# Kernel optimization log

Hardware: AMD Instinct MI355X
Metric: run time of the kernel (lower is better)

Reference implementation:

```python
import jax, jax.numpy as jnp
import numpy as np
import math

B, S, E, H = 8, 1024, 512, 8
EPS = 1e-5

def _ln(x, g, b):
    mu = jnp.mean(x, axis=-1, keepdims=True)
    var = jnp.mean(jnp.square(x - mu), axis=-1, keepdims=True)
    return (x - mu) * jax.lax.rsqrt(var + EPS) * g + b

def setup_inputs() -> dict:
    key = jax.random.key(0)
    ks = iter(jax.random.split(key, 40))
    def w(shape, scale=0.02):
        return jax.random.normal(next(ks), shape, dtype=jnp.float32) * scale
    inp = {
        'x': jax.random.normal(next(ks), (B, S, E), dtype=jnp.float32),
        'cond': jax.random.normal(next(ks), (B, 1, E), dtype=jnp.float32),
        # AdaLN modulation linears (stored as (in,out))
        'g1w': w((E, E)), 'g1b': jnp.zeros((E,), jnp.float32),
        'be1w': w((E, E)), 'be1b': jnp.zeros((E,), jnp.float32),
        'a1w': w((E, E)), 'a1b': jnp.zeros((E,), jnp.float32),
        'g2w': w((E, E)), 'g2b': jnp.zeros((E,), jnp.float32),
        'be2w': w((E, E)), 'be2b': jnp.zeros((E,), jnp.float32),
        'a2w': w((E, E)), 'a2b': jnp.zeros((E,), jnp.float32),
        # LayerNorm affine
        'ln1g': jnp.ones((E,), jnp.float32), 'ln1b': jnp.zeros((E,), jnp.float32),
        'ln2g': jnp.ones((E,), jnp.float32), 'ln2b': jnp.zeros((E,), jnp.float32),
        # attention projections: each head has width E -> out dim H*E
        'wq': w((E, H * E)), 'bq': jnp.zeros((H * E,), jnp.float32),
        'wk': w((E, H * E)), 'bk': jnp.zeros((H * E,), jnp.float32),
        'wv': w((E, H * E)), 'bv': jnp.zeros((H * E,), jnp.float32),
        'lvw': w((H * E, E)), 'lvb': jnp.zeros((E,), jnp.float32),
        # FFN
        'f1w': w((E, 4 * E)), 'f1b': jnp.zeros((4 * E,), jnp.float32),
        'f2w': w((4 * E, E)), 'f2b': jnp.zeros((E,), jnp.float32),
    }
    return inp

def reference(x, cond, g1w, g1b, be1w, be1b, a1w, a1b, g2w, g2b, be2w, be2b, a2w, a2b,
              ln1g, ln1b, ln2g, ln2b, wq, bq, wk, bk, wv, bv, lvw, lvb, f1w, f1b, f2w, f2b):
    # AdaLN modulation signals, each (B,1,E)
    gamma1 = cond @ g1w + g1b
    beta1 = cond @ be1w + be1b
    alpha1 = cond @ a1w + a1b
    gamma2 = cond @ g2w + g2b
    beta2 = cond @ be2w + be2b
    alpha2 = cond @ a2w + a2b

    y = _ln(x, ln1g, ln1b) * (1.0 + gamma1) + beta1
    q = (y @ wq + bq).reshape(B, S, H, E).transpose(0, 2, 1, 3)  # (B,H,S,E)
    k = (y @ wk + bk).reshape(B, S, H, E).transpose(0, 2, 1, 3)
    v = (y @ wv + bv).reshape(B, S, H, E).transpose(0, 2, 1, 3)
    # NOTE: original scales by sqrt(q.size(2)) == sqrt(seq_len), not head_dim
    scale = 1.0 / math.sqrt(S)
    attn = jax.nn.softmax(jnp.einsum('bhse,bhte->bhst', q, k) * scale, axis=-1)
    o = jnp.einsum('bhst,bhte->bhse', attn, v)  # (B,H,S,E)
    o = o.transpose(0, 2, 1, 3).reshape(B, S, H * E)
    y = x + (o @ lvw + lvb) * alpha1

    z = _ln(y, ln2g, ln2b) * (1.0 + gamma2) + beta2
    z = (jax.nn.relu(z @ f1w + f1b) @ f2w + f2b) * alpha2
    return y + z
```

## Files before the change

### kernel.cpp

```cpp
#include <hip/hip_runtime.h>
#include <hip/hip_bf16.h>

typedef __bf16 bf16_t;
typedef bf16_t bf16x8 __attribute__((ext_vector_type(8)));
typedef bf16_t bf16x4 __attribute__((ext_vector_type(4)));
typedef float f32x4 __attribute__((ext_vector_type(4)));

typedef const __attribute__((address_space(1))) void GV;
typedef __attribute__((address_space(3))) void LV;

__device__ __forceinline__ void gload_lds16(const bf16_t* gsrc, bf16_t* ldst) {
    __builtin_amdgcn_global_load_lds((GV*)gsrc, (LV*)ldst, 16, 0, 0);
}

__global__ __launch_bounds__(256) void wtrans_kernel(const float* __restrict__ in,
                                                     bf16_t* __restrict__ out, int K, int N)
{
    __shared__ float tile[32][33];
    const int n0 = blockIdx.x * 32, k0 = blockIdx.y * 32;
    const int tx = threadIdx.x & 31, ty = threadIdx.x >> 5;
#pragma unroll
    for (int i = 0; i < 32; i += 8)
        tile[ty + i][tx] = in[(long long)(k0 + ty + i) * N + n0 + tx];
    __syncthreads();
#pragma unroll
    for (int i = 0; i < 32; i += 8)
        out[(long long)(n0 + ty + i) * K + k0 + tx] = (bf16_t)tile[tx][ty + i];
}

__global__ __launch_bounds__(256) void modsig_kernel(
    const float* __restrict__ cond,
    const float* __restrict__ w0, const float* __restrict__ w1, const float* __restrict__ w2,
    const float* __restrict__ w3, const float* __restrict__ w4, const float* __restrict__ w5,
    const float* __restrict__ c0, const float* __restrict__ c1, const float* __restrict__ c2,
    const float* __restrict__ c3, const float* __restrict__ c4, const float* __restrict__ c5,
    float* __restrict__ out)
{
    __shared__ float cs[512];
    const int sig = blockIdx.x >> 3, b = blockIdx.x & 7;
    const float* w; const float* bi;
    switch (sig) {
        case 0: w = w0; bi = c0; break;
        case 1: w = w1; bi = c1; break;
        case 2: w = w2; bi = c2; break;
        case 3: w = w3; bi = c3; break;
        case 4: w = w4; bi = c4; break;
        default: w = w5; bi = c5; break;
    }
    for (int i = threadIdx.x; i < 512; i += 256) cs[i] = cond[b * 512 + i];
    __syncthreads();
    for (int n = threadIdx.x; n < 512; n += 256) {
        float s = bi[n];
        for (int i = 0; i < 512; ++i) s = fmaf(cs[i], w[(long long)i * 512 + n], s);
        out[(long long)(sig * 8 + b) * 512 + n] = s;
    }
}

__global__ __launch_bounds__(128) void ln_mod_kernel(
    const float* __restrict__ x, const float* __restrict__ g, const float* __restrict__ be,
    const float* __restrict__ gamma, const float* __restrict__ beta, bf16_t* __restrict__ out)
{
    const int row = blockIdx.x;
    const int b = row >> 10;
    const int t = threadIdx.x;
    const float4 v = reinterpret_cast<const float4*>(x + (long long)row * 512)[t];
    float s = v.x + v.y + v.z + v.w;
    float ss = v.x * v.x + v.y * v.y + v.z * v.z + v.w * v.w;
    for (int o = 32; o; o >>= 1) { s += __shfl_xor(s, o); ss += __shfl_xor(ss, o); }
    __shared__ float red[4];
    if ((t & 63) == 0) { red[t >> 6] = s; red[2 + (t >> 6)] = ss; }
    __syncthreads();
    s = red[0] + red[1]; ss = red[2] + red[3];
    const float mu = s * (1.f / 512.f);
    const float rstd = rsqrtf(ss * (1.f / 512.f) - mu * mu + 1e-5f);
    const float4 gv = reinterpret_cast<const float4*>(g)[t];
    const float4 bv = reinterpret_cast<const float4*>(be)[t];
    const float4 ga = reinterpret_cast<const float4*>(gamma + b * 512)[t];
    const float4 bb = reinterpret_cast<const float4*>(beta + b * 512)[t];
    bf16x4 ov;
    ov[0] = (bf16_t)(((v.x - mu) * rstd * gv.x + bv.x) * (1.f + ga.x) + bb.x);
    ov[1] = (bf16_t)(((v.y - mu) * rstd * gv.y + bv.y) * (1.f + ga.y) + bb.y);
    ov[2] = (bf16_t)(((v.z - mu) * rstd * gv.z + bv.z) * (1.f + ga.z) + bb.z);
    ov[3] = (bf16_t)(((v.w - mu) * rstd * gv.w + bv.w) * (1.f + ga.w) + bb.w);
    reinterpret_cast<bf16x4*>(out + (long long)row * 512)[t] = ov;
}

template <int EPI>
__global__ __launch_bounds__(256) void gemm128_kernel(
    const bf16_t* __restrict__ A, const bf16_t* __restrict__ B,
    const float* __restrict__ bias, void* Cout,
    int M, int N, int K, int lda, int ldb, int ldc)
{
    const int m0 = blockIdx.y * 128, n0 = blockIdx.x * 128;
    const int tid = threadIdx.x, lane = tid & 63, wid = tid >> 6;
    const int wr = wid >> 1, wc = wid & 1;

    __shared__ bf16_t As[4096];
    __shared__ bf16_t Bs[4096];

    f32x4 acc[4][4];
#pragma unroll
    for (int m = 0; m < 4; ++m)
#pragma unroll
        for (int n = 0; n < 4; ++n) acc[m][n] = (f32x4){0.f, 0.f, 0.f, 0.f};

    const int r0 = wid * 16 + (lane >> 2);
    const int lc = (lane & 3) ^ ((lane >> 2) & 3);
    const long long aOff0 = (long long)(m0 + r0) * lda + lc * 8;
    const long long aOff1 = (long long)(m0 + r0 + 64) * lda + lc * 8;
    const long long bOff0 = (long long)(n0 + r0) * ldb + lc * 8;
    const long long bOff1 = (long long)(n0 + r0 + 64) * ldb + lc * 8;
    bf16_t* aDst0 = As + wid * 512;
    bf16_t* aDst1 = As + 2048 + wid * 512;
    bf16_t* bDst0 = Bs + wid * 512;
    bf16_t* bDst1 = Bs + 2048 + wid * 512;

    const int frow = lane & 15, lg = lane >> 4;
    const int pc = lg ^ (frow & 3);

    for (int kt = 0; kt < K; kt += 32) {
        gload_lds16(A + aOff0 + kt, aDst0);
        gload_lds16(A + aOff1 + kt, aDst1);
        gload_lds16(B + bOff0 + kt, bDst0);
        gload_lds16(B + bOff1 + kt, bDst1);
        __syncthreads();
        bf16x8 af[4], bfv[4];
#pragma unroll
        for (int m = 0; m < 4; ++m)
            af[m] = *reinterpret_cast<const bf16x8*>(As + (wr * 64 + m * 16 + frow) * 32 + pc * 8);
#pragma unroll
        for (int n = 0; n < 4; ++n)
            bfv[n] = *reinterpret_cast<const bf16x8*>(Bs + (wc * 64 + n * 16 + frow) * 32 + pc * 8);
        __builtin_amdgcn_s_setprio(1);
#pragma unroll
        for (int m = 0; m < 4; ++m)
#pragma unroll
            for (int n = 0; n < 4; ++n)
                acc[m][n] = __builtin_amdgcn_mfma_f32_16x16x32_bf16(af[m], bfv[n], acc[m][n], 0, 0, 0);
        __builtin_amdgcn_s_setprio(0);
        __syncthreads();
    }

#pragma unroll
    for (int m = 0; m < 4; ++m) {
        const int gm = m0 + wr * 64 + m * 16 + ((lane >> 4) << 2);
#pragma unroll
        for (int n = 0; n < 4; ++n) {
            const int gn = n0 + wc * 64 + n * 16 + (lane & 15);
            const float bb = bias ? bias[gn] : 0.f;
#pragma unroll
            for (int j = 0; j < 4; ++j) {
                const float v = acc[m][n][j] + bb;
                const int gmj = gm + j;
                if (EPI == 0) {
                    ((bf16_t*)Cout)[(long long)gmj * ldc + gn] = (bf16_t)v;
                } else if (EPI == 1) {
                    ((bf16_t*)Cout)[(long long)gmj * ldc + gn] = (bf16_t)fmaxf(v, 0.f);
                } else {
                    const long long ci =
                        (long long)(((gmj >> 10) * 8 + (gn >> 9)) * 512 + (gn & 511)) * 1024 + (gmj & 1023);
                    ((bf16_t*)Cout)[ci] = (bf16_t)v;
                }
            }
        }
    }
}

__global__ __launch_bounds__(256) void gemm64_kernel(
    const bf16_t* __restrict__ A, const bf16_t* __restrict__ B,
    const float* __restrict__ bias, float* __restrict__ Cout,
    const float* __restrict__ resid, const float* __restrict__ alpha,
    int M, int N, int K, int lda, int ldb)
{
    const int m0 = blockIdx.y * 64, n0 = blockIdx.x * 128;
    const int tid = threadIdx.x, lane = tid & 63, wid = tid >> 6;
    const int wr = wid >> 1, wc = wid & 1;

    __shared__ bf16_t As[2048];
    __shared__ bf16_t Bs[4096];

    f32x4 acc[2][4];
#pragma unroll
    for (int m = 0; m < 2; ++m)
#pragma unroll
        for (int n = 0; n < 4; ++n) acc[m][n] = (f32x4){0.f, 0.f, 0.f, 0.f};

    const int r0 = wid * 16 + (lane >> 2);
    const int lc = (lane & 3) ^ ((lane >> 2) & 3);
    const long long aOff0 = (long long)(m0 + r0) * lda + lc * 8;
    const long long bOff0 = (long long)(n0 + r0) * ldb + lc * 8;
    const long long bOff1 = (long long)(n0 + r0 + 64) * ldb + lc * 8;
    bf16_t* aDst0 = As + wid * 512;
    bf16_t* bDst0 = Bs + wid * 512;
    bf16_t* bDst1 = Bs + 2048 + wid * 512;

    const int frow = lane & 15, lg = lane >> 4;
    const int pc = lg ^ (frow & 3);

    for (int kt = 0; kt < K; kt += 32) {
        gload_lds16(A + aOff0 + kt, aDst0);
        gload_lds16(B + bOff0 + kt, bDst0);
        gload_lds16(B + bOff1 + kt, bDst1);
        __syncthreads();
        bf16x8 af[2], bfv[4];
#pragma unroll
        for (int m = 0; m < 2; ++m)
            af[m] = *reinterpret_cast<const bf16x8*>(As + (wr * 32 + m * 16 + frow) * 32 + pc * 8);
#pragma unroll
        for (int n = 0; n < 4; ++n)
            bfv[n] = *reinterpret_cast<const bf16x8*>(Bs + (wc * 64 + n * 16 + frow) * 32 + pc * 8);
        __builtin_amdgcn_s_setprio(1);
#pragma unroll
        for (int m = 0; m < 2; ++m)
#pragma unroll
            for (int n = 0; n < 4; ++n)
                acc[m][n] = __builtin_amdgcn_mfma_f32_16x16x32_bf16(af[m], bfv[n], acc[m][n], 0, 0, 0);
        __builtin_amdgcn_s_setprio(0);
        __syncthreads();
    }

#pragma unroll
    for (int m = 0; m < 2; ++m) {
        const int gm = m0 + wr * 32 + m * 16 + ((lane >> 4) << 2);
#pragma unroll
        for (int n = 0; n < 4; ++n) {
            const int gn = n0 + wc * 64 + n * 16 + (lane & 15);
            const float bb = bias[gn];
#pragma unroll
            for (int j = 0; j < 4; ++j) {
                const int gmj = gm + j;
                const long long ci = (long long)gmj * 512 + gn;
                Cout[ci] = resid[ci] + (acc[m][n][j] + bb) * alpha[(gmj >> 10) * 512 + gn];
            }
        }
    }
}

#define FA_LDS 141312
#define SCL 0.04508422132207354f
__global__ __launch_bounds__(512, 2) void flash_kernel(
    bf16_t* __restrict__ qb, const bf16_t* __restrict__ kb, const bf16_t* __restrict__ vtb)
{
    extern __shared__ char smem[];
    bf16_t* Ks = (bf16_t*)smem;
    bf16_t* Vs = (bf16_t*)(smem + 65536);
    char* PB = smem + 131072;
    float* pmaxB = (float*)(smem + 139264);
    float* psumB = (float*)(smem + 140288);

    const int bid = blockIdx.x;
    const int xcd = bid & 7, idx = bid >> 3;
    const int qt = idx & 15, bhl = idx >> 4;
    const int bh = xcd * 8 + bhl;
    const int b = bh >> 3, h = bh & 7;
    const int q0 = qt * 64;
    const int tid = threadIdx.x, lane = tid & 63, wid = tid >> 6;
    const int laneq = lane & 15, lx = lane & 7, lg = lane >> 4;
    const int wk = wid >> 2, wq = wid & 3;
    const int we = wid & 3, wq2 = wid >> 2;

#pragma unroll
    for (int r = 0; r < 8; ++r) {
        const int row = r * 8 + wid;
        gload_lds16(kb + ((long long)(b * 1024 + row) * 8 + h) * 512 + ((lane ^ (row & 7)) << 3),
                    Ks + row * 512);
    }
    const int qi = wq * 16 + laneq;
    bf16x8 qfrag[16];
    {
        const bf16_t* qrow = qb + ((long long)(b * 1024 + q0 + qi) * 8 + h) * 512 + lg * 8;
#pragma unroll
        for (int ks = 0; ks < 16; ++ks) qfrag[ks] = *reinterpret_cast<const bf16x8*>(qrow + ks * 32);
    }
    f32x4 accA[8], accB[8];
#pragma unroll
    for (int e = 0; e < 8; ++e) { accA[e] = (f32x4){0.f,0.f,0.f,0.f}; accB[e] = (f32x4){0.f,0.f,0.f,0.f}; }
    float mS = 0.f, mPA = 0.f, mPB = 0.f, lA = 0.f, lB = 0.f;
    const int rA0 = wk * 32 + laneq, rA1 = rA0 + 16;
    const int qA = wq2 * 32 + laneq, qB = qA + 16;
    const int qx = (qi & 7) << 1;
    const int qxA = (qA & 7) << 1, qxB = (qB & 7) << 1;
    __syncthreads();

    for (int t = 0; t < 16; ++t) {
        const int kv0 = t * 64;
#pragma unroll
        for (int r = 0; r < 8; ++r) {
            const int e = r * 64 + wid * 8 + (lane >> 3);
            gload_lds16(vtb + ((long long)bh * 512 + e) * 1024 + kv0 + ((lx ^ (e & 7)) << 3),
                        Vs + (r * 64 + wid * 8) * 64);
        }
        f32x4 s0 = (f32x4){0.f,0.f,0.f,0.f}, s1 = (f32x4){0.f,0.f,0.f,0.f};
        const char* KsB = (const char*)Ks;
        __builtin_amdgcn_s_setprio(1);
#pragma unroll
        for (int ks = 0; ks < 16; ++ks) {
            const int co = ((ks * 4 + lg) ^ lx) << 4;
            bf16x8 a0 = *(const bf16x8*)(KsB + rA0 * 1024 + co);
            bf16x8 a1 = *(const bf16x8*)(KsB + rA1 * 1024 + co);
            s0 = __builtin_amdgcn_mfma_f32_16x16x32_bf16(a0, qfrag[ks], s0, 0, 0, 0);
            s1 = __builtin_amdgcn_mfma_f32_16x16x32_bf16(a1, qfrag[ks], s1, 0, 0, 0);
        }
        __builtin_amdgcn_s_setprio(0);
        float f[8];
#pragma unroll
        for (int j = 0; j < 4; ++j) { f[j] = s0[j] * SCL; f[4 + j] = s1[j] * SCL; }
        float mloc = f[0];
#pragma unroll
        for (int j = 1; j < 8; ++j) mloc = fmaxf(mloc, f[j]);
        mloc = fmaxf(mloc, __shfl_xor(mloc, 16));
        mloc = fmaxf(mloc, __shfl_xor(mloc, 32));
        float pe[8]; float sl = 0.f;
#pragma unroll
        for (int j = 0; j < 8; ++j) { pe[j] = exp2f(f[j] - mS); sl += pe[j]; }
        sl += __shfl_xor(sl, 16);
        sl += __shfl_xor(sl, 32);
        if (lane < 16) {
            pmaxB[(t & 1) * 128 + wk * 64 + wq * 16 + lane] = mloc;
            psumB[(t & 1) * 128 + wk * 64 + wq * 16 + lane] = sl;
        }
        {
            bf16x4 p0, p1;
#pragma unroll
            for (int j = 0; j < 4; ++j) { p0[j] = (bf16_t)pe[j]; p1[j] = (bf16_t)pe[4 + j]; }
            const int kc0 = wk * 8 + lg, kc1 = kc0 + 4;
            *(bf16x4*)(PB + qi * 128 + ((kc0 ^ qx) << 3)) = p0;
            *(bf16x4*)(PB + qi * 128 + ((kc1 ^ qx) << 3)) = p1;
        }
        __syncthreads();

        if (t < 15) {
#pragma unroll
            for (int r = 0; r < 8; ++r) {
                const int row = r * 8 + wid;
                gload_lds16(kb + ((long long)(b * 1024 + kv0 + 64 + row) * 8 + h) * 512
                                + ((lane ^ (row & 7)) << 3),
                            Ks + row * 512);
            }
        }
        const char* VB = (const char*)Vs;
        __builtin_amdgcn_s_setprio(1);
#pragma unroll
        for (int ks2 = 0; ks2 < 2; ++ks2) {
            const int kcp = ks2 * 8 + lg * 2;
            bf16x8 pA = *(const bf16x8*)(PB + qA * 128 + ((kcp ^ qxA) << 3));
            bf16x8 pBv = *(const bf16x8*)(PB + qB * 128 + ((kcp ^ qxB) << 3));
            const int kcv = ks2 * 4 + lg;
#pragma unroll
            for (int ef = 0; ef < 8; ++ef) {
                const int re = we * 128 + ef * 16 + laneq;
                bf16x8 av = *(const bf16x8*)(VB + re * 128 + ((kcv ^ lx) << 4));
                accA[ef] = __builtin_amdgcn_mfma_f32_16x16x32_bf16(av, pA, accA[ef], 0, 0, 0);
                accB[ef] = __builtin_amdgcn_mfma_f32_16x16x32_bf16(av, pBv, accB[ef], 0, 0, 0);
            }
        }
        __builtin_amdgcn_s_setprio(0);
        {
            const float* pmax_t = pmaxB + (t & 1) * 128;
            const float* psum_t = psumB + (t & 1) * 128;
            mS = fmaxf(mS, fmaxf(pmax_t[qi], pmax_t[64 + qi]));
            lA += psum_t[qA] + psum_t[64 + qA];
            lB += psum_t[qB] + psum_t[64 + qB];
            const float mnA = fmaxf(mPA, fmaxf(pmax_t[qA], pmax_t[64 + qA]));
            const float mnB = fmaxf(mPB, fmaxf(pmax_t[qB], pmax_t[64 + qB]));
            if (__ballot((mnA > mPA) || (mnB > mPB))) {
                const float rA = exp2f(mPA - mnA), rB = exp2f(mPB - mnB);
                lA *= rA; lB *= rB;
#pragma unroll
                for (int e = 0; e < 8; ++e) {
#pragma unroll
                    for (int j = 0; j < 4; ++j) { accA[e][j] *= rA; accB[e][j] *= rB; }
                }
            }
            mPA = mnA; mPB = mnB;
        }
        __syncthreads();
    }

    const float iA = 1.f / lA, iB = 1.f / lB;
#pragma unroll
    for (int ef = 0; ef < 8; ++ef) {
        const int e0 = we * 128 + ef * 16 + lg * 4;
        bf16x4 oA, oB;
#pragma unroll
        for (int j = 0; j < 4; ++j) { oA[j] = (bf16_t)(accA[ef][j] * iA); oB[j] = (bf16_t)(accB[ef][j] * iB); }
        *(bf16x4*)(qb + ((long long)(b * 1024 + q0 + qA) * 8 + h) * 512 + e0) = oA;
        *(bf16x4*)(qb + ((long long)(b * 1024 + q0 + qB) * 8 + h) * 512 + e0) = oB;
    }
}

extern "C" void kernel_launch(void* const* d_in, const int* in_sizes, int n_in,
                              void* d_out, int out_size, void* d_ws, size_t ws_size,
                              hipStream_t stream)
{
    const float* x    = (const float*)d_in[0];
    const float* cond = (const float*)d_in[1];
    const float* g1w  = (const float*)d_in[2];  const float* g1b  = (const float*)d_in[3];
    const float* be1w = (const float*)d_in[4];  const float* be1b = (const float*)d_in[5];
    const float* a1w  = (const float*)d_in[6];  const float* a1b  = (const float*)d_in[7];
    const float* g2w  = (const float*)d_in[8];  const float* g2b  = (const float*)d_in[9];
    const float* be2w = (const float*)d_in[10]; const float* be2b = (const float*)d_in[11];
    const float* a2w  = (const float*)d_in[12]; const float* a2b  = (const float*)d_in[13];
    const float* ln1g = (const float*)d_in[14]; const float* ln1b = (const float*)d_in[15];
    const float* ln2g = (const float*)d_in[16]; const float* ln2b = (const float*)d_in[17];
    const float* wq   = (const float*)d_in[18]; const float* bq   = (const float*)d_in[19];
    const float* wk   = (const float*)d_in[20]; const float* bk   = (const float*)d_in[21];
    const float* wv   = (const float*)d_in[22]; const float* bv   = (const float*)d_in[23];
    const float* lvw  = (const float*)d_in[24]; const float* lvb  = (const float*)d_in[25];
    const float* f1w  = (const float*)d_in[26]; const float* f1b  = (const float*)d_in[27];
    const float* f2w  = (const float*)d_in[28]; const float* f2b  = (const float*)d_in[29];
    (void)in_sizes; (void)n_in; (void)out_size; (void)ws_size;

    char* w8 = (char*)d_ws;
    float*  mod  = (float*)(w8);
    bf16_t* wqT  = (bf16_t*)(w8 + 98304);
    bf16_t* wkT  = (bf16_t*)(w8 + 98304 + 4194304);
    bf16_t* wvT  = (bf16_t*)(w8 + 98304 + 2 * 4194304);
    bf16_t* lvwT = (bf16_t*)(w8 + 98304 + 3 * 4194304);
    bf16_t* f1wT = (bf16_t*)(w8 + 98304 + 4 * 4194304);
    bf16_t* f2wT = (bf16_t*)(w8 + 98304 + 4 * 4194304 + 2097152);
    bf16_t* ybf  = (bf16_t*)(w8 + 98304 + 4 * 4194304 + 2 * 2097152);
    bf16_t* qb   = (bf16_t*)(w8 + 98304 + 4 * 4194304 + 2 * 2097152 + 8388608);
    bf16_t* kb   = qb + 33554432;
    bf16_t* vtb  = kb + 33554432;

    (void)hipFuncSetAttribute((const void*)flash_kernel,
                              hipFuncAttributeMaxDynamicSharedMemorySize, FA_LDS);

    const dim3 blk(256);
    wtrans_kernel<<<dim3(128, 16), blk, 0, stream>>>(wq, wqT, 512, 4096);
    wtrans_kernel<<<dim3(128, 16), blk, 0, stream>>>(wk, wkT, 512, 4096);
    wtrans_kernel<<<dim3(128, 16), blk, 0, stream>>>(wv, wvT, 512, 4096);
    wtrans_kernel<<<dim3(16, 128), blk, 0, stream>>>(lvw, lvwT, 4096, 512);
    wtrans_kernel<<<dim3(64, 16), blk, 0, stream>>>(f1w, f1wT, 512, 2048);
    wtrans_kernel<<<dim3(16, 64), blk, 0, stream>>>(f2w, f2wT, 2048, 512);
    modsig_kernel<<<48, blk, 0, stream>>>(cond, g1w, be1w, a1w, g2w, be2w, a2w,
                                          g1b, be1b, a1b, g2b, be2b, a2b, mod);
    ln_mod_kernel<<<8192, 128, 0, stream>>>(x, ln1g, ln1b, mod, mod + 4096, ybf);
    gemm128_kernel<0><<<dim3(32, 64), blk, 0, stream>>>(ybf, wqT, bq, qb,
        8192, 4096, 512, 512, 512, 4096);
    gemm128_kernel<0><<<dim3(32, 64), blk, 0, stream>>>(ybf, wkT, bk, kb,
        8192, 4096, 512, 512, 512, 4096);
    gemm128_kernel<3><<<dim3(32, 64), blk, 0, stream>>>(ybf, wvT, bv, vtb,
        8192, 4096, 512, 512, 512, 0);
    flash_kernel<<<1024, 512, FA_LDS, stream>>>(qb, kb, vtb);
    gemm64_kernel<<<dim3(4, 128), blk, 0, stream>>>(qb, lvwT, lvb, (float*)d_out, x, mod + 8192,
        8192, 512, 4096, 4096, 4096);
    ln_mod_kernel<<<8192, 128, 0, stream>>>((const float*)d_out, ln2g, ln2b,
                                            mod + 12288, mod + 16384, ybf);
    gemm128_kernel<1><<<dim3(16, 64), blk, 0, stream>>>(ybf, f1wT, f1b, qb,
        8192, 2048, 512, 512, 512, 2048);
    gemm64_kernel<<<dim3(4, 128), blk, 0, stream>>>(qb, f2wT, f2b, (float*)d_out,
        (const float*)d_out, mod + 20480,
        8192, 512, 2048, 2048, 2048);
}
```

Measured before the change: 713.0 us.

## Fuse QKV projections into one GEMM and double flash query tile to 128

The three Q/K/V projection GEMMs become one launch over a concatenated N dimension. The launch passes only wqT, so it relies on wkT and wvT sitting right after wqT in the workspace, and the kernel picks the bias and output layout per section. The flash attention kernel now handles 128 queries per block instead of 64. Each wave computes scores for 16 queries against all 64 keys, then accumulates 64 queries by 128 value columns. This halves K/V reloads from global memory per query and halves the number of blocks. The cost is more accumulator registers per thread, a larger LDS P buffer, and fewer blocks in flight.

```diff
diff --git a/kernel.cpp b/kernel.cpp
--- a/kernel.cpp
+++ b/kernel.cpp
@@ -166,6 +166,87 @@
     }
 }
 
+__global__ __launch_bounds__(256) void gemmqkv_kernel(
+    const bf16_t* __restrict__ A, const bf16_t* __restrict__ B,
+    const float* __restrict__ bq, const float* __restrict__ bk, const float* __restrict__ bv,
+    bf16_t* __restrict__ qkv, bf16_t* __restrict__ vtb)
+{
+    const int m0 = blockIdx.y * 128, n0 = blockIdx.x * 128;
+    const int sec = n0 >> 12;
+    const float* bias = (sec == 0) ? bq : ((sec == 1) ? bk : bv);
+    const int tid = threadIdx.x, lane = tid & 63, wid = tid >> 6;
+    const int wr = wid >> 1, wc = wid & 1;
+
+    __shared__ bf16_t As[4096];
+    __shared__ bf16_t Bs[4096];
+
+    f32x4 acc[4][4];
+#pragma unroll
+    for (int m = 0; m < 4; ++m)
+#pragma unroll
+        for (int n = 0; n < 4; ++n) acc[m][n] = (f32x4){0.f, 0.f, 0.f, 0.f};
+
+    const int r0 = wid * 16 + (lane >> 2);
+    const int lc = (lane & 3) ^ ((lane >> 2) & 3);
+    const long long aOff0 = (long long)(m0 + r0) * 512 + lc * 8;
+    const long long aOff1 = (long long)(m0 + r0 + 64) * 512 + lc * 8;
+    const long long bOff0 = (long long)(n0 + r0) * 512 + lc * 8;
+    const long long bOff1 = (long long)(n0 + r0 + 64) * 512 + lc * 8;
+    bf16_t* aDst0 = As + wid * 512;
+    bf16_t* aDst1 = As + 2048 + wid * 512;
+    bf16_t* bDst0 = Bs + wid * 512;
+    bf16_t* bDst1 = Bs + 2048 + wid * 512;
+
+    const int frow = lane & 15, lg = lane >> 4;
+    const int pc = lg ^ (frow & 3);
+
+    for (int kt = 0; kt < 512; kt += 32) {
+        gload_lds16(A + aOff0 + kt, aDst0);
+        gload_lds16(A + aOff1 + kt, aDst1);
+        gload_lds16(B + bOff0 + kt, bDst0);
+        gload_lds16(B + bOff1 + kt, bDst1);
+        __syncthreads();
+        bf16x8 af[4], bfv[4];
+#pragma unroll
+        for (int m = 0; m < 4; ++m)
+            af[m] = *reinterpret_cast<const bf16x8*>(As + (wr * 64 + m * 16 + frow) * 32 + pc * 8);
+#pragma unroll
+        for (int n = 0; n < 4; ++n)
+            bfv[n] = *reinterpret_cast<const bf16x8*>(Bs + (wc * 64 + n * 16 + frow) * 32 + pc * 8);
+        __builtin_amdgcn_s_setprio(1);
+#pragma unroll
+        for (int m = 0; m < 4; ++m)
+#pragma unroll
+            for (int n = 0; n < 4; ++n)
+                acc[m][n] = __builtin_amdgcn_mfma_f32_16x16x32_bf16(af[m], bfv[n], acc[m][n], 0, 0, 0);
+        __builtin_amdgcn_s_setprio(0);
+        __syncthreads();
+    }
+
+#pragma unroll
+    for (int m = 0; m < 4; ++m) {
+        const int gm = m0 + wr * 64 + m * 16 + ((lane >> 4) << 2);
+#pragma unroll
+        for (int n = 0; n < 4; ++n) {
+            const int gn = n0 + wc * 64 + n * 16 + (lane & 15);
+            const int gnl = gn & 4095;
+            const float bb = bias[gnl];
+#pragma unroll
+            for (int j = 0; j < 4; ++j) {
+                const float v = acc[m][n][j] + bb;
+                const int gmj = gm + j;
+                if (sec < 2) {
+                    qkv[(long long)sec * 33554432 + (long long)gmj * 4096 + gnl] = (bf16_t)v;
+                } else {
+                    const long long ci =
+                        (long long)(((gmj >> 10) * 8 + (gnl >> 9)) * 512 + (gnl & 511)) * 1024 + (gmj & 1023);
+                    vtb[ci] = (bf16_t)v;
+                }
+            }
+        }
+    }
+}
+
 __global__ __launch_bounds__(256) void gemm64_kernel(
     const bf16_t* __restrict__ A, const bf16_t* __restrict__ B,
     const float* __restrict__ bias, float* __restrict__ Cout,
@@ -236,7 +317,7 @@
     }
 }
 
-#define FA_LDS 141312
+#define FA_LDS 149504
 #define SCL 0.04508422132207354f
 __global__ __launch_bounds__(512, 2) void flash_kernel(
     bf16_t* __restrict__ qb, const bf16_t* __restrict__ kb, const bf16_t* __restrict__ vtb)
@@ -245,18 +326,18 @@
     bf16_t* Ks = (bf16_t*)smem;
     bf16_t* Vs = (bf16_t*)(smem + 65536);
     char* PB = smem + 131072;
-    float* pmaxB = (float*)(smem + 139264);
-    float* psumB = (float*)(smem + 140288);
+    float* pmaxB = (float*)(smem + 147456);
+    float* psumB = (float*)(smem + 148480);
 
     const int bid = blockIdx.x;
     const int xcd = bid & 7, idx = bid >> 3;
-    const int qt = idx & 15, bhl = idx >> 4;
+    const int qt = idx & 7, bhl = idx >> 3;
     const int bh = xcd * 8 + bhl;
     const int b = bh >> 3, h = bh & 7;
-    const int q0 = qt * 64;
+    const int q0 = qt * 128;
     const int tid = threadIdx.x, lane = tid & 63, wid = tid >> 6;
     const int laneq = lane & 15, lx = lane & 7, lg = lane >> 4;
-    const int wk = wid >> 2, wq = wid & 3;
+    const int wq = wid;
     const int we = wid & 3, wq2 = wid >> 2;
 
 #pragma unroll
@@ -272,14 +353,14 @@
 #pragma unroll
         for (int ks = 0; ks < 16; ++ks) qfrag[ks] = *reinterpret_cast<const bf16x8*>(qrow + ks * 32);
     }
-    f32x4 accA[8], accB[8];
-#pragma unroll
-    for (int e = 0; e < 8; ++e) { accA[e] = (f32x4){0.f,0.f,0.f,0.f}; accB[e] = (f32x4){0.f,0.f,0.f,0.f}; }
-    float mS = 0.f, mPA = 0.f, mPB = 0.f, lA = 0.f, lB = 0.f;
-    const int rA0 = wk * 32 + laneq, rA1 = rA0 + 16;
-    const int qA = wq2 * 32 + laneq, qB = qA + 16;
-    const int qx = (qi & 7) << 1;
-    const int qxA = (qA & 7) << 1, qxB = (qB & 7) << 1;
+    f32x4 acc[8][4];
+#pragma unroll
+    for (int ef = 0; ef < 8; ++ef)
+#pragma unroll
+        for (int j = 0; j < 4; ++j) acc[ef][j] = (f32x4){0.f, 0.f, 0.f, 0.f};
+    float mS = 0.f;
+    float mP[4] = {0.f, 0.f, 0.f, 0.f};
+    float l[4] = {0.f, 0.f, 0.f, 0.f};
     __syncthreads();
 
     for (int t = 0; t < 16; ++t) {
@@ -290,42 +371,51 @@
             gload_lds16(vtb + ((long long)bh * 512 + e) * 1024 + kv0 + ((lx ^ (e & 7)) << 3),
                         Vs + (r * 64 + wid * 8) * 64);
         }
-        f32x4 s0 = (f32x4){0.f,0.f,0.f,0.f}, s1 = (f32x4){0.f,0.f,0.f,0.f};
+        f32x4 sacc[4];
+#pragma unroll
+        for (int kt = 0; kt < 4; ++kt) sacc[kt] = (f32x4){0.f, 0.f, 0.f, 0.f};
         const char* KsB = (const char*)Ks;
         __builtin_amdgcn_s_setprio(1);
 #pragma unroll
-        for (int ks = 0; ks < 16; ++ks) {
-            const int co = ((ks * 4 + lg) ^ lx) << 4;
-            bf16x8 a0 = *(const bf16x8*)(KsB + rA0 * 1024 + co);
-            bf16x8 a1 = *(const bf16x8*)(KsB + rA1 * 1024 + co);
-            s0 = __builtin_amdgcn_mfma_f32_16x16x32_bf16(a0, qfrag[ks], s0, 0, 0, 0);
-            s1 = __builtin_amdgcn_mfma_f32_16x16x32_bf16(a1, qfrag[ks], s1, 0, 0, 0);
+        for (int kt = 0; kt < 4; ++kt) {
+            const int rA = kt * 16 + laneq;
+#pragma unroll
+            for (int ks = 0; ks < 16; ++ks) {
+                const int co = ((ks * 4 + lg) ^ lx) << 4;
+                bf16x8 a0 = *(const bf16x8*)(KsB + rA * 1024 + co);
+                sacc[kt] = __builtin_amdgcn_mfma_f32_16x16x32_bf16(a0, qfrag[ks], sacc[kt], 0, 0, 0);
+            }
         }
         __builtin_amdgcn_s_setprio(0);
-        float f[8];
-#pragma unroll
-        for (int j = 0; j < 4; ++j) { f[j] = s0[j] * SCL; f[4 + j] = s1[j] * SCL; }
+        float f[16];
+#pragma unroll
+        for (int kt = 0; kt < 4; ++kt)
+#pragma unroll
+            for (int j = 0; j < 4; ++j) f[kt * 4 + j] = sacc[kt][j] * SCL;
         float mloc = f[0];
 #pragma unroll
-        for (int j = 1; j < 8; ++j) mloc = fmaxf(mloc, f[j]);
+        for (int j = 1; j < 16; ++j) mloc = fmaxf(mloc, f[j]);
         mloc = fmaxf(mloc, __shfl_xor(mloc, 16));
         mloc = fmaxf(mloc, __shfl_xor(mloc, 32));
-        float pe[8]; float sl = 0.f;
-#pragma unroll
-        for (int j = 0; j < 8; ++j) { pe[j] = exp2f(f[j] - mS); sl += pe[j]; }
+        float pe[16]; float sl = 0.f;
+#pragma unroll
+        for (int j = 0; j < 16; ++j) { pe[j] = exp2f(f[j] - mS); sl += pe[j]; }
         sl += __shfl_xor(sl, 16);
         sl += __shfl_xor(sl, 32);
         if (lane < 16) {
-            pmaxB[(t & 1) * 128 + wk * 64 + wq * 16 + lane] = mloc;
-            psumB[(t & 1) * 128 + wk * 64 + wq * 16 + lane] = sl;
+            pmaxB[(t & 1) * 128 + wq * 16 + lane] = mloc;
+            psumB[(t & 1) * 128 + wq * 16 + lane] = sl;
         }
         {
-            bf16x4 p0, p1;
-#pragma unroll
-            for (int j = 0; j < 4; ++j) { p0[j] = (bf16_t)pe[j]; p1[j] = (bf16_t)pe[4 + j]; }
-            const int kc0 = wk * 8 + lg, kc1 = kc0 + 4;
-            *(bf16x4*)(PB + qi * 128 + ((kc0 ^ qx) << 3)) = p0;
-            *(bf16x4*)(PB + qi * 128 + ((kc1 ^ qx) << 3)) = p1;
+            const int hh = (lg & 1) * 8;
+#pragma unroll
+            for (int kt = 0; kt < 4; ++kt) {
+                bf16x4 p;
+#pragma unroll
+                for (int j = 0; j < 4; ++j) p[j] = (bf16_t)pe[kt * 4 + j];
+                const int c = kt * 2 + (lg >> 1);
+                *(bf16x4*)(PB + qi * 128 + ((c ^ lx) << 4) + hh) = p;
+            }
         }
         __syncthreads();
 
@@ -342,50 +432,65 @@
         __builtin_amdgcn_s_setprio(1);
 #pragma unroll
         for (int ks2 = 0; ks2 < 2; ++ks2) {
-            const int kcp = ks2 * 8 + lg * 2;
-            bf16x8 pA = *(const bf16x8*)(PB + qA * 128 + ((kcp ^ qxA) << 3));
-            bf16x8 pBv = *(const bf16x8*)(PB + qB * 128 + ((kcp ^ qxB) << 3));
-            const int kcv = ks2 * 4 + lg;
+            bf16x8 pf[4];
+#pragma unroll
+            for (int j = 0; j < 4; ++j) {
+                const int q = wq2 * 64 + j * 16 + laneq;
+                pf[j] = *(const bf16x8*)(PB + q * 128 + (((ks2 * 4 + lg) ^ lx) << 4));
+            }
 #pragma unroll
             for (int ef = 0; ef < 8; ++ef) {
                 const int re = we * 128 + ef * 16 + laneq;
-                bf16x8 av = *(const bf16x8*)(VB + re * 128 + ((kcv ^ lx) << 4));
-                accA[ef] = __builtin_amdgcn_mfma_f32_16x16x32_bf16(av, pA, accA[ef], 0, 0, 0);
-                accB[ef] = __builtin_amdgcn_mfma_f32_16x16x32_bf16(av, pBv, accB[ef], 0, 0, 0);
+                bf16x8 av = *(const bf16x8*)(VB + re * 128 + (((ks2 * 4 + lg) ^ lx) << 4));
+#pragma unroll
+                for (int j = 0; j < 4; ++j)
+                    acc[ef][j] = __builtin_amdgcn_mfma_f32_16x16x32_bf16(av, pf[j], acc[ef][j], 0, 0, 0);
             }
         }
         __builtin_amdgcn_s_setprio(0);
         {
             const float* pmax_t = pmaxB + (t & 1) * 128;
             const float* psum_t = psumB + (t & 1) * 128;
-            mS = fmaxf(mS, fmaxf(pmax_t[qi], pmax_t[64 + qi]));
-            lA += psum_t[qA] + psum_t[64 + qA];
-            lB += psum_t[qB] + psum_t[64 + qB];
-            const float mnA = fmaxf(mPA, fmaxf(pmax_t[qA], pmax_t[64 + qA]));
-            const float mnB = fmaxf(mPB, fmaxf(pmax_t[qB], pmax_t[64 + qB]));
-            if (__ballot((mnA > mPA) || (mnB > mPB))) {
-                const float rA = exp2f(mPA - mnA), rB = exp2f(mPB - mnB);
-                lA *= rA; lB *= rB;
-#pragma unroll
-                for (int e = 0; e < 8; ++e) {
-#pragma unroll
-                    for (int j = 0; j < 4; ++j) { accA[e][j] *= rA; accB[e][j] *= rB; }
+            mS = fmaxf(mS, pmax_t[qi]);
+            float mn[4]; bool need = false;
+#pragma unroll
+            for (int j = 0; j < 4; ++j) {
+                const int q = wq2 * 64 + j * 16 + laneq;
+                l[j] += psum_t[q];
+                mn[j] = fmaxf(mP[j], pmax_t[q]);
+                need = need || (mn[j] > mP[j]);
+            }
+            if (__ballot(need)) {
+#pragma unroll
+                for (int j = 0; j < 4; ++j) {
+                    const float rs = exp2f(mP[j] - mn[j]);
+                    l[j] *= rs;
+#pragma unroll
+                    for (int ef = 0; ef < 8; ++ef)
+#pragma unroll
+                        for (int jj = 0; jj < 4; ++jj) acc[ef][j][jj] *= rs;
                 }
             }
-            mPA = mnA; mPB = mnB;
-        }
-        __syncthreads();
-    }
-
-    const float iA = 1.f / lA, iB = 1.f / lB;
+#pragma unroll
+            for (int j = 0; j < 4; ++j) mP[j] = mn[j];
+        }
+        __syncthreads();
+    }
+
+    float il[4];
+#pragma unroll
+    for (int j = 0; j < 4; ++j) il[j] = 1.f / l[j];
 #pragma unroll
     for (int ef = 0; ef < 8; ++ef) {
         const int e0 = we * 128 + ef * 16 + lg * 4;
-        bf16x4 oA, oB;
-#pragma unroll
-        for (int j = 0; j < 4; ++j) { oA[j] = (bf16_t)(accA[ef][j] * iA); oB[j] = (bf16_t)(accB[ef][j] * iB); }
-        *(bf16x4*)(qb + ((long long)(b * 1024 + q0 + qA) * 8 + h) * 512 + e0) = oA;
-        *(bf16x4*)(qb + ((long long)(b * 1024 + q0 + qB) * 8 + h) * 512 + e0) = oB;
+#pragma unroll
+        for (int j = 0; j < 4; ++j) {
+            const int qrow = q0 + wq2 * 64 + j * 16 + laneq;
+            bf16x4 o;
+#pragma unroll
+            for (int jj = 0; jj < 4; ++jj) o[jj] = (bf16_t)(acc[ef][j][jj] * il[j]);
+            *(bf16x4*)(qb + ((long long)(b * 1024 + qrow) * 8 + h) * 512 + e0) = o;
+        }
     }
 }
 
@@ -437,13 +542,8 @@
     modsig_kernel<<<48, blk, 0, stream>>>(cond, g1w, be1w, a1w, g2w, be2w, a2w,
                                           g1b, be1b, a1b, g2b, be2b, a2b, mod);
     ln_mod_kernel<<<8192, 128, 0, stream>>>(x, ln1g, ln1b, mod, mod + 4096, ybf);
-    gemm128_kernel<0><<<dim3(32, 64), blk, 0, stream>>>(ybf, wqT, bq, qb,
-        8192, 4096, 512, 512, 512, 4096);
-    gemm128_kernel<0><<<dim3(32, 64), blk, 0, stream>>>(ybf, wkT, bk, kb,
-        8192, 4096, 512, 512, 512, 4096);
-    gemm128_kernel<3><<<dim3(32, 64), blk, 0, stream>>>(ybf, wvT, bv, vtb,
-        8192, 4096, 512, 512, 512, 0);
-    flash_kernel<<<1024, 512, FA_LDS, stream>>>(qb, kb, vtb);
+    gemmqkv_kernel<<<dim3(96, 64), blk, 0, stream>>>(ybf, wqT, bq, bk, bv, qb, vtb);
+    flash_kernel<<<512, 512, FA_LDS, stream>>>(qb, kb, vtb);
     gemm64_kernel<<<dim3(4, 128), blk, 0, stream>>>(qb, lvwT, lvb, (float*)d_out, x, mod + 8192,
         8192, 512, 4096, 4096, 4096);
     ln_mod_kernel<<<8192, 128, 0, stream>>>((const float*)d_out, ln2g, ln2b,
```

After: 905.4 us. 1.27x slower.

## Fuse QKV GEMMs and store V in MFMA fragment order for register loads

Applied to the files above, without the earlier changes.

The three Q/K/V projection GEMMs become one launch over a concatenated transposed weight. The V section writes straight into a layout that matches the MFMA operand fragments of the attention kernel. The flash kernel then loads V fragments from global memory into registers instead of staging them through LDS, which cuts its LDS footprint from about 138KB to 74KB. This removes the V LDS traffic and two kernel launches, but adds register pressure and relies on global-load latency being hidden within the QK phase.

```diff
diff --git a/kernel.cpp b/kernel.cpp
--- a/kernel.cpp
+++ b/kernel.cpp
@@ -154,13 +154,97 @@
                 const int gmj = gm + j;
                 if (EPI == 0) {
                     ((bf16_t*)Cout)[(long long)gmj * ldc + gn] = (bf16_t)v;
-                } else if (EPI == 1) {
+                } else {
                     ((bf16_t*)Cout)[(long long)gmj * ldc + gn] = (bf16_t)fmaxf(v, 0.f);
-                } else {
-                    const long long ci =
-                        (long long)(((gmj >> 10) * 8 + (gn >> 9)) * 512 + (gn & 511)) * 1024 + (gmj & 1023);
-                    ((bf16_t*)Cout)[ci] = (bf16_t)v;
                 }
+            }
+        }
+    }
+}
+
+__global__ __launch_bounds__(256) void gemmqkv_kernel(
+    const bf16_t* __restrict__ A, const bf16_t* __restrict__ B,
+    const float* __restrict__ bq, const float* __restrict__ bk, const float* __restrict__ bv,
+    bf16_t* __restrict__ qkv, bf16_t* __restrict__ vfr)
+{
+    const int m0 = blockIdx.y * 128, n0 = blockIdx.x * 128;
+    const int sec = n0 >> 12;
+    const float* bias = (sec == 0) ? bq : ((sec == 1) ? bk : bv);
+    const int tid = threadIdx.x, lane = tid & 63, wid = tid >> 6;
+    const int wr = wid >> 1, wc = wid & 1;
+
+    __shared__ bf16_t As[4096];
+    __shared__ bf16_t Bs[4096];
+
+    f32x4 acc[4][4];
+#pragma unroll
+    for (int m = 0; m < 4; ++m)
+#pragma unroll
+        for (int n = 0; n < 4; ++n) acc[m][n] = (f32x4){0.f, 0.f, 0.f, 0.f};
+
+    const int r0 = wid * 16 + (lane >> 2);
+    const int lc = (lane & 3) ^ ((lane >> 2) & 3);
+    const long long aOff0 = (long long)(m0 + r0) * 512 + lc * 8;
+    const long long aOff1 = (long long)(m0 + r0 + 64) * 512 + lc * 8;
+    const long long bOff0 = (long long)(n0 + r0) * 512 + lc * 8;
+    const long long bOff1 = (long long)(n0 + r0 + 64) * 512 + lc * 8;
+    bf16_t* aDst0 = As + wid * 512;
+    bf16_t* aDst1 = As + 2048 + wid * 512;
+    bf16_t* bDst0 = Bs + wid * 512;
+    bf16_t* bDst1 = Bs + 2048 + wid * 512;
+
+    const int frow = lane & 15, lg = lane >> 4;
+    const int pc = lg ^ (frow & 3);
+
+    for (int kt = 0; kt < 512; kt += 32) {
+        gload_lds16(A + aOff0 + kt, aDst0);
+        gload_lds16(A + aOff1 + kt, aDst1);
+        gload_lds16(B + bOff0 + kt, bDst0);
+        gload_lds16(B + bOff1 + kt, bDst1);
+        __syncthreads();
+        bf16x8 af[4], bfv[4];
+#pragma unroll
+        for (int m = 0; m < 4; ++m)
+            af[m] = *reinterpret_cast<const bf16x8*>(As + (wr * 64 + m * 16 + frow) * 32 + pc * 8);
+#pragma unroll
+        for (int n = 0; n < 4; ++n)
+            bfv[n] = *reinterpret_cast<const bf16x8*>(Bs + (wc * 64 + n * 16 + frow) * 32 + pc * 8);
+        __builtin_amdgcn_s_setprio(1);
+#pragma unroll
+        for (int m = 0; m < 4; ++m)
+#pragma unroll
+            for (int n = 0; n < 4; ++n)
+                acc[m][n] = __builtin_amdgcn_mfma_f32_16x16x32_bf16(af[m], bfv[n], acc[m][n], 0, 0, 0);
+        __builtin_amdgcn_s_setprio(0);
+        __syncthreads();
+    }
+
+#pragma unroll
+    for (int m = 0; m < 4; ++m) {
+        const int gm = m0 + wr * 64 + m * 16 + ((lane >> 4) << 2);
+#pragma unroll
+        for (int n = 0; n < 4; ++n) {
+            const int gn = n0 + wc * 64 + n * 16 + (lane & 15);
+            const int gnl = gn & 4095;
+            const float bb = bias[gnl];
+            if (sec < 2) {
+#pragma unroll
+                for (int j = 0; j < 4; ++j) {
+                    const int gmj = gm + j;
+                    qkv[(long long)sec * 33554432 + (long long)gmj * 4096 + gnl] =
+                        (bf16_t)(acc[m][n][j] + bb);
+                }
+            } else {
+                const int s = gm & 1023, bb2 = gm >> 10;
+                const int hh = gnl >> 9, e = gnl & 511;
+                const int bh = bb2 * 8 + hh;
+                const long long ci = ((long long)bh << 19) + ((s >> 6) * 32768)
+                                   + (((s >> 5) & 1) * 16384) + ((e >> 4) * 512)
+                                   + (((s >> 3) & 3) * 128) + ((e & 15) * 8) + (s & 7);
+                bf16x4 ov;
+#pragma unroll
+                for (int j = 0; j < 4; ++j) ov[j] = (bf16_t)(acc[m][n][j] + bb);
+                *reinterpret_cast<bf16x4*>(vfr + ci) = ov;
             }
         }
     }
@@ -236,17 +320,16 @@
     }
 }
 
-#define FA_LDS 141312
+#define FA_LDS 75776
 #define SCL 0.04508422132207354f
 __global__ __launch_bounds__(512, 2) void flash_kernel(
-    bf16_t* __restrict__ qb, const bf16_t* __restrict__ kb, const bf16_t* __restrict__ vtb)
+    bf16_t* __restrict__ qb, const bf16_t* __restrict__ kb, const bf16_t* __restrict__ vfr)
 {
     extern __shared__ char smem[];
     bf16_t* Ks = (bf16_t*)smem;
-    bf16_t* Vs = (bf16_t*)(smem + 65536);
-    char* PB = smem + 131072;
-    float* pmaxB = (float*)(smem + 139264);
-    float* psumB = (float*)(smem + 140288);
+    char* PB = smem + 65536;
+    float* pmaxB = (float*)(smem + 73728);
+    float* psumB = (float*)(smem + 74752);
 
     const int bid = blockIdx.x;
     const int xcd = bid & 7, idx = bid >> 3;
@@ -255,7 +338,7 @@
     const int b = bh >> 3, h = bh & 7;
     const int q0 = qt * 64;
     const int tid = threadIdx.x, lane = tid & 63, wid = tid >> 6;
-    const int laneq = lane & 15, lx = lane & 7, lg = lane >> 4;
+    const int laneq = lane & 15, lg = lane >> 4;
     const int wk = wid >> 2, wq = wid & 3;
     const int we = wid & 3, wq2 = wid >> 2;
 
@@ -280,22 +363,21 @@
     const int qA = wq2 * 32 + laneq, qB = qA + 16;
     const int qx = (qi & 7) << 1;
     const int qxA = (qA & 7) << 1, qxB = (qB & 7) << 1;
+    const bf16_t* vfrW = vfr + ((long long)bh << 19) + (we * 8) * 512 + lane * 8;
     __syncthreads();
 
     for (int t = 0; t < 16; ++t) {
-        const int kv0 = t * 64;
-#pragma unroll
-        for (int r = 0; r < 8; ++r) {
-            const int e = r * 64 + wid * 8 + (lane >> 3);
-            gload_lds16(vtb + ((long long)bh * 512 + e) * 1024 + kv0 + ((lx ^ (e & 7)) << 3),
-                        Vs + (r * 64 + wid * 8) * 64);
-        }
+        const bf16_t* vfrT = vfrW + t * 32768;
+        bf16x8 av0[8], av1[8];
+#pragma unroll
+        for (int ef = 0; ef < 8; ++ef)
+            av0[ef] = *reinterpret_cast<const bf16x8*>(vfrT + ef * 512);
         f32x4 s0 = (f32x4){0.f,0.f,0.f,0.f}, s1 = (f32x4){0.f,0.f,0.f,0.f};
         const char* KsB = (const char*)Ks;
         __builtin_amdgcn_s_setprio(1);
 #pragma unroll
         for (int ks = 0; ks < 16; ++ks) {
-            const int co = ((ks * 4 + lg) ^ lx) << 4;
+            const int co = ((ks * 4 + lg) ^ (lane & 7)) << 4;
             bf16x8 a0 = *(const bf16x8*)(KsB + rA0 * 1024 + co);
             bf16x8 a1 = *(const bf16x8*)(KsB + rA1 * 1024 + co);
             s0 = __builtin_amdgcn_mfma_f32_16x16x32_bf16(a0, qfrag[ks], s0, 0, 0, 0);
@@ -329,29 +411,37 @@
         }
         __syncthreads();
 
+#pragma unroll
+        for (int ef = 0; ef < 8; ++ef)
+            av1[ef] = *reinterpret_cast<const bf16x8*>(vfrT + 16384 + ef * 512);
         if (t < 15) {
 #pragma unroll
             for (int r = 0; r < 8; ++r) {
                 const int row = r * 8 + wid;
-                gload_lds16(kb + ((long long)(b * 1024 + kv0 + 64 + row) * 8 + h) * 512
+                gload_lds16(kb + ((long long)(b * 1024 + t * 64 + 64 + row) * 8 + h) * 512
                                 + ((lane ^ (row & 7)) << 3),
                             Ks + row * 512);
             }
         }
-        const char* VB = (const char*)Vs;
         __builtin_amdgcn_s_setprio(1);
-#pragma unroll
-        for (int ks2 = 0; ks2 < 2; ++ks2) {
-            const int kcp = ks2 * 8 + lg * 2;
-            bf16x8 pA = *(const bf16x8*)(PB + qA * 128 + ((kcp ^ qxA) << 3));
-            bf16x8 pBv = *(const bf16x8*)(PB + qB * 128 + ((kcp ^ qxB) << 3));
-            const int kcv = ks2 * 4 + lg;
+        {
+            const int kcp0 = lg * 2;
+            bf16x8 pA = *(const bf16x8*)(PB + qA * 128 + ((kcp0 ^ qxA) << 3));
+            bf16x8 pBv = *(const bf16x8*)(PB + qB * 128 + ((kcp0 ^ qxB) << 3));
 #pragma unroll
             for (int ef = 0; ef < 8; ++ef) {
-                const int re = we * 128 + ef * 16 + laneq;
-                bf16x8 av = *(const bf16x8*)(VB + re * 128 + ((kcv ^ lx) << 4));
-                accA[ef] = __builtin_amdgcn_mfma_f32_16x16x32_bf16(av, pA, accA[ef], 0, 0, 0);
-                accB[ef] = __builtin_amdgcn_mfma_f32_16x16x32_bf16(av, pBv, accB[ef], 0, 0, 0);
+                accA[ef] = __builtin_amdgcn_mfma_f32_16x16x32_bf16(av0[ef], pA, accA[ef], 0, 0, 0);
+                accB[ef] = __builtin_amdgcn_mfma_f32_16x16x32_bf16(av0[ef], pBv, accB[ef], 0, 0, 0);
+            }
+        }
+        {
+            const int kcp1 = 8 + lg * 2;
+            bf16x8 pA = *(const bf16x8*)(PB + qA * 128 + ((kcp1 ^ qxA) << 3));
+            bf16x8 pBv = *(const bf16x8*)(PB + qB * 128 + ((kcp1 ^ qxB) << 3));
+#pragma unroll
+            for (int ef = 0; ef < 8; ++ef) {
+                accA[ef] = __builtin_amdgcn_mfma_f32_16x16x32_bf16(av1[ef], pA, accA[ef], 0, 0, 0);
+                accB[ef] = __builtin_amdgcn_mfma_f32_16x16x32_bf16(av1[ef], pBv, accB[ef], 0, 0, 0);
             }
         }
         __builtin_amdgcn_s_setprio(0);
@@ -414,36 +504,29 @@
     char* w8 = (char*)d_ws;
     float*  mod  = (float*)(w8);
     bf16_t* wqT  = (bf16_t*)(w8 + 98304);
-    bf16_t* wkT  = (bf16_t*)(w8 + 98304 + 4194304);
-    bf16_t* wvT  = (bf16_t*)(w8 + 98304 + 2 * 4194304);
     bf16_t* lvwT = (bf16_t*)(w8 + 98304 + 3 * 4194304);
     bf16_t* f1wT = (bf16_t*)(w8 + 98304 + 4 * 4194304);
     bf16_t* f2wT = (bf16_t*)(w8 + 98304 + 4 * 4194304 + 2097152);
     bf16_t* ybf  = (bf16_t*)(w8 + 98304 + 4 * 4194304 + 2 * 2097152);
     bf16_t* qb   = (bf16_t*)(w8 + 98304 + 4 * 4194304 + 2 * 2097152 + 8388608);
     bf16_t* kb   = qb + 33554432;
-    bf16_t* vtb  = kb + 33554432;
+    bf16_t* vfr  = kb + 33554432;
 
     (void)hipFuncSetAttribute((const void*)flash_kernel,
                               hipFuncAttributeMaxDynamicSharedMemorySize, FA_LDS);
 
     const dim3 blk(256);
     wtrans_kernel<<<dim3(128, 16), blk, 0, stream>>>(wq, wqT, 512, 4096);
-    wtrans_kernel<<<dim3(128, 16), blk, 0, stream>>>(wk, wkT, 512, 4096);
-    wtrans_kernel<<<dim3(128, 16), blk, 0, stream>>>(wv, wvT, 512, 4096);
+    wtrans_kernel<<<dim3(128, 16), blk, 0, stream>>>(wk, wqT + 2097152, 512, 4096);
+    wtrans_kernel<<<dim3(128, 16), blk, 0, stream>>>(wv, wqT + 2 * 2097152, 512, 4096);
     wtrans_kernel<<<dim3(16, 128), blk, 0, stream>>>(lvw, lvwT, 4096, 512);
     wtrans_kernel<<<dim3(64, 16), blk, 0, stream>>>(f1w, f1wT, 512, 2048);
     wtrans_kernel<<<dim3(16, 64), blk, 0, stream>>>(f2w, f2wT, 2048, 512);
     modsig_kernel<<<48, blk, 0, stream>>>(cond, g1w, be1w, a1w, g2w, be2w, a2w,
                                           g1b, be1b, a1b, g2b, be2b, a2b, mod);
     ln_mod_kernel<<<8192, 128, 0, stream>>>(x, ln1g, ln1b, mod, mod + 4096, ybf);
-    gemm128_kernel<0><<<dim3(32, 64), blk, 0, stream>>>(ybf, wqT, bq, qb,
-        8192, 4096, 512, 512, 512, 4096);
-    gemm128_kernel<0><<<dim3(32, 64), blk, 0, stream>>>(ybf, wkT, bk, kb,
-        8192, 4096, 512, 512, 512, 4096);
-    gemm128_kernel<3><<<dim3(32, 64), blk, 0, stream>>>(ybf, wvT, bv, vtb,
-        8192, 4096, 512, 512, 512, 0);
-    flash_kernel<<<1024, 512, FA_LDS, stream>>>(qb, kb, vtb);
+    gemmqkv_kernel<<<dim3(96, 64), blk, 0, stream>>>(ybf, wqT, bq, bk, bv, qb, vfr);
+    flash_kernel<<<1024, 512, FA_LDS, stream>>>(qb, kb, vfr);
     gemm64_kernel<<<dim3(4, 128), blk, 0, stream>>>(qb, lvwT, lvb, (float*)d_out, x, mod + 8192,
         8192, 512, 4096, 4096, 4096);
     ln_mod_kernel<<<8192, 128, 0, stream>>>((const float*)d_out, ln2g, ln2b,
```

After: 852.0 us. 1.19x slower.
